# Optimization experiments

Measured on AMD Instinct MI355X. Metric: run time of the kernel, lower is better.

## Reference

```python
import jax, jax.numpy as jnp
import numpy as np

FEATS = 512   # F, forced by groups=512
K = 8         # kernel_size arg (number of shifted taps)
L = 3         # lag
CK = 3        # actual Conv1d kernel width
OUT_CH = K * FEATS * L  # 12288


def setup_inputs() -> dict:
    key = jax.random.key(0)
    k1, k2, k3 = jax.random.split(key, 3)
    M, T = 4, 1024
    x = jax.random.normal(k1, (M, T, FEATS), dtype=jnp.float32)
    # grouped conv: out_channels=12288, in_channels/groups = 512/512 = 1, width 3
    conv_w = jax.random.normal(k2, (OUT_CH, 1, CK), dtype=jnp.float32) * 0.1
    conv_b = jax.random.normal(k3, (OUT_CH,), dtype=jnp.float32) * 0.1
    return {"x": x, "conv_w": conv_w, "conv_b": conv_b}


def reference(x, conv_w, conv_b):
    M, T, F = x.shape
    # causal grouped conv: left-pad CK-1, feature_group_count = F
    xc = jnp.transpose(x, (0, 2, 1))  # (M, F, T)
    y = jax.lax.conv_general_dilated(
        xc, conv_w, window_strides=(1,), padding=[(CK - 1, 0)],
        dimension_numbers=("NCH", "OIH", "NCH"), feature_group_count=F)
    y = y + conv_b[None, :, None]                   # (M, OUT_CH, T)
    y = jnp.transpose(y, (0, 2, 1)).reshape(M, T, F, K, L)

    t = jnp.arange(T)
    lag_slices = []
    for l in range(L):
        taps = []
        for i in range(K):
            s = i + l
            # NOTE: original torch code rolls along the FEATURE axis (dim 2 of (M,T,F))
            z = jnp.roll(y[:, :, :, i, l], s, axis=2)      # (M, T, F)
            # ... but zeros the first s TIME steps (faithful reproduction)
            z = jnp.where((t >= s)[None, :, None], z, 0.0)
            taps.append(z)
        lag_slices.append(jnp.stack(taps, axis=-1))        # (M, T, F, K)
    x_new = jnp.stack(lag_slices, axis=0)                   # (L, M, T, F, K)
    x_new = x_new.reshape(L * M, T, F, K)
    return jnp.transpose(x_new, (2, 1, 0, 3))               # (F, T, L*M, K)
```

## Files before the change

### kernel.cpp

```cpp
#include <hip/hip_runtime.h>


typedef float f32x4 __attribute__((ext_vector_type(4)));

#define NF 512
#define NT 1024
#define TT 64
#define XROW 12
#define NROWS 66
#define XM 808

__global__ __launch_bounds__(256) void caconv_kernel(
    const float* __restrict__ x,
    const float* __restrict__ w,
    const float* __restrict__ b,
    float* __restrict__ out)
{
    __shared__ float x_lds[4 * XM];
    __shared__ float w_lds[72];
    __shared__ float b_lds[24];

    const int tid = threadIdx.x;
    const int f   = blockIdx.x >> 4;
    const int t0  = (blockIdx.x & 15) * TT;

    if (tid < 72) {
        const int l = tid / 24, r = tid - l * 24, tap = r >> 3, k = r & 7;
        const int fs = (f - k - l + NF) & (NF - 1);
        w_lds[tid] = w[(fs * 24 + k * 3 + l) * 3 + tap];
    } else if (tid < 96) {
        const int j = tid - 72, l = j >> 3, k = j & 7;
        const int fs = (f - k - l + NF) & (NF - 1);
        b_lds[j] = b[fs * 24 + k * 3 + l];
    }

    for (int i = tid; i < 4 * NROWS * XROW; i += 256) {
        const int fi  = i % 12;
        const int row = i / 12;
        const int tt  = row % NROWS;
        const int m   = row / NROWS;
        const int tg  = t0 - 2 + tt;
        const int fs  = (f - 11 + fi + NF) & (NF - 1);
        float v = 0.0f;
        if (tg >= 0) v = x[((m << 10) + tg) * NF + fs];
        x_lds[m * XM + tt * XROW + fi] = v;
    }
    __syncthreads();

    float* const outb = out + ((size_t)f * NT + t0) * 96;

    const int kh = tid & 1;
    const int k0 = kh << 2;
    int q     = tid >> 1;
    int t_off = q / 12;
    int lm    = q - t_off * 12;

#pragma unroll 1
    for (int j = 0; j < 6; ++j) {
        const int l = lm >> 2, m = lm & 3;

        const float* wp = w_lds + l * 24 + k0;
        const f32x4 w0 = *(const f32x4*)(wp);
        const f32x4 w1 = *(const f32x4*)(wp + 8);
        const f32x4 w2 = *(const f32x4*)(wp + 16);
        f32x4 acc = *(const f32x4*)(b_lds + l * 8 + k0);

        const float* xp = x_lds + m * XM + t_off * XROW + (8 - l - k0);

        {
            const float r0 = xp[0], r1 = xp[1], r2 = xp[2], r3 = xp[3];
            acc[0] += w0[0] * r3; acc[1] += w0[1] * r2;
            acc[2] += w0[2] * r1; acc[3] += w0[3] * r0;
        }
        {
            const float r0 = xp[12], r1 = xp[13], r2 = xp[14], r3 = xp[15];
            acc[0] += w1[0] * r3; acc[1] += w1[1] * r2;
            acc[2] += w1[2] * r1; acc[3] += w1[3] * r0;
        }
        {
            const float r0 = xp[24], r1 = xp[25], r2 = xp[26], r3 = xp[27];
            acc[0] += w2[0] * r3; acc[1] += w2[1] * r2;
            acc[2] += w2[2] * r1; acc[3] += w2[3] * r0;
        }

        if (t0 == 0 && t_off < 9) {
#pragma unroll
            for (int kk = 0; kk < 4; ++kk)
                if (t_off < k0 + kk + l) acc[kk] = 0.0f;
        }

        *(f32x4*)(outb + (t_off * 12 + lm) * 8 + k0) = acc;

        lm += 8; t_off += 10;
        if (lm >= 12) { lm -= 12; ++t_off; }
    }
}

extern "C" void kernel_launch(void* const* d_in, const int* in_sizes, int n_in,
                              void* d_out, int out_size, void* d_ws, size_t ws_size,
                              hipStream_t stream)
{
    const float* x = (const float*)d_in[0];
    const float* w = (const float*)d_in[1];
    const float* b = (const float*)d_in[2];
    float* out = (float*)d_out;

    const int grid = NF * (NT / TT);
    caconv_kernel<<<grid, 256, 0, stream>>>(x, w, b, out);
}
```

Measured before the change: 48.21 us.

## Make blocks persistent over time tiles with double-buffered register-prefetched staging

Each block now covers 512 time steps as 8 tiles instead of one 64-step tile, which shrinks the grid from 8192 to 1024 blocks. The next tile's x window is prefetched into registers while the current tile is computed from a double-buffered LDS slab. The staged feature window is narrowed from 12 to 10 columns and the gather addresses are precomputed once per block. The aim is to hide global load latency behind compute and to amortize per-block weight and bias setup, at the cost of fewer blocks in flight and more registers.

```diff
diff --git a/kernel.cpp b/kernel.cpp
--- a/kernel.cpp
+++ b/kernel.cpp
@@ -6,93 +6,135 @@
 #define NF 512
 #define NT 1024
 #define TT 64
-#define XROW 12
+#define XROW 10
 #define NROWS 66
-#define XM 808
+#define XM 668
+#define SLAB (4 * XM)
+#define NSTG (4 * NROWS * XROW)
+#define NIT 11
+#define DUMMY (SLAB - 1)
 
-__global__ __launch_bounds__(256) void caconv_kernel(
+__global__ __launch_bounds__(256, 4) void caconv_kernel(
     const float* __restrict__ x,
     const float* __restrict__ w,
     const float* __restrict__ b,
     float* __restrict__ out)
 {
-    __shared__ float x_lds[4 * XM];
+    __shared__ float x_lds[2 * SLAB];
     __shared__ float w_lds[72];
     __shared__ float b_lds[24];
 
-    const int tid = threadIdx.x;
-    const int f   = blockIdx.x >> 4;
-    const int t0  = (blockIdx.x & 15) * TT;
+    const int tid   = threadIdx.x;
+    const int f     = blockIdx.x >> 1;
+    const int tbase = (blockIdx.x & 1) << 9;
 
     if (tid < 72) {
-        const int l = tid / 24, r = tid - l * 24, tap = r >> 3, k = r & 7;
+        const int l = tid / 24, rr = tid - l * 24, tap = rr >> 3, k = rr & 7;
         const int fs = (f - k - l + NF) & (NF - 1);
         w_lds[tid] = w[(fs * 24 + k * 3 + l) * 3 + tap];
     } else if (tid < 96) {
-        const int j = tid - 72, l = j >> 3, k = j & 7;
+        const int jj = tid - 72, l = jj >> 3, k = jj & 7;
         const int fs = (f - k - l + NF) & (NF - 1);
-        b_lds[j] = b[fs * 24 + k * 3 + l];
+        b_lds[jj] = b[fs * 24 + k * 3 + l];
     }
 
-    for (int i = tid; i < 4 * NROWS * XROW; i += 256) {
-        const int fi  = i % 12;
-        const int row = i / 12;
-        const int tt  = row % NROWS;
-        const int m   = row / NROWS;
-        const int tg  = t0 - 2 + tt;
-        const int fs  = (f - 11 + fi + NF) & (NF - 1);
+    int goff[NIT], pk[NIT];
+#pragma unroll
+    for (int it = 0; it < NIT; ++it) {
+        const int i = tid + it * 256;
+        if (i < NSTG) {
+            const int fi = i % 10, row = i / 10;
+            const int tt = row % 66, m = row / 66;
+            const int fs = (f - 9 + fi + NF) & (NF - 1);
+            goff[it] = ((tt - 2) << 9) + fs;
+            pk[it]   = ((m * XM + tt * XROW + fi) << 2) | m;
+        } else {
+            goff[it] = -(1 << 30);
+            pk[it]   = DUMMY << 2;
+        }
+    }
+
+    float r[NIT];
+
+#pragma unroll
+    for (int it = 0; it < NIT; ++it) {
+        const int g = goff[it] + (tbase << 9);
         float v = 0.0f;
-        if (tg >= 0) v = x[((m << 10) + tg) * NF + fs];
-        x_lds[m * XM + tt * XROW + fi] = v;
+        if (g >= 0) v = x[g + ((pk[it] & 3) << 19)];
+        r[it] = v;
     }
+#pragma unroll
+    for (int it = 0; it < NIT; ++it) x_lds[pk[it] >> 2] = r[it];
     __syncthreads();
 
-    float* const outb = out + ((size_t)f * NT + t0) * 96;
-
-    const int kh = tid & 1;
-    const int k0 = kh << 2;
-    int q     = tid >> 1;
-    int t_off = q / 12;
-    int lm    = q - t_off * 12;
+    const int k0     = (tid & 1) << 2;
+    const int q0     = tid >> 1;
+    const int t_off0 = q0 / 12;
+    const int lm0    = q0 - t_off0 * 12;
 
 #pragma unroll 1
-    for (int j = 0; j < 6; ++j) {
-        const int l = lm >> 2, m = lm & 3;
+    for (int j = 0; j < 8; ++j) {
+        const int t0 = tbase + j * TT;
+        const float* bufr = x_lds + (j & 1) * SLAB;
+        float* bufw       = x_lds + ((j & 1) ^ 1) * SLAB;
 
-        const float* wp = w_lds + l * 24 + k0;
-        const f32x4 w0 = *(const f32x4*)(wp);
-        const f32x4 w1 = *(const f32x4*)(wp + 8);
-        const f32x4 w2 = *(const f32x4*)(wp + 16);
-        f32x4 acc = *(const f32x4*)(b_lds + l * 8 + k0);
-
-        const float* xp = x_lds + m * XM + t_off * XROW + (8 - l - k0);
-
-        {
-            const float r0 = xp[0], r1 = xp[1], r2 = xp[2], r3 = xp[3];
-            acc[0] += w0[0] * r3; acc[1] += w0[1] * r2;
-            acc[2] += w0[2] * r1; acc[3] += w0[3] * r0;
-        }
-        {
-            const float r0 = xp[12], r1 = xp[13], r2 = xp[14], r3 = xp[15];
-            acc[0] += w1[0] * r3; acc[1] += w1[1] * r2;
-            acc[2] += w1[2] * r1; acc[3] += w1[3] * r0;
-        }
-        {
-            const float r0 = xp[24], r1 = xp[25], r2 = xp[26], r3 = xp[27];
-            acc[0] += w2[0] * r3; acc[1] += w2[1] * r2;
-            acc[2] += w2[2] * r1; acc[3] += w2[3] * r0;
+        if (j < 7) {
+            const int t1s = (t0 + TT) << 9;
+#pragma unroll
+            for (int it = 0; it < NIT; ++it) {
+                const int g = goff[it] + t1s;
+                float v = 0.0f;
+                if (g >= 0) v = x[g + ((pk[it] & 3) << 19)];
+                r[it] = v;
+            }
         }
 
-        if (t0 == 0 && t_off < 9) {
+        float* const outb = out + (size_t)((f << 10) + t0) * 96;
+        int t_off = t_off0, lm = lm0;
+#pragma unroll 1
+        for (int c = 0; c < 6; ++c) {
+            const int l = lm >> 2, m = lm & 3;
+
+            const float* wp = w_lds + l * 24 + k0;
+            const f32x4 w0 = *(const f32x4*)(wp);
+            const f32x4 w1 = *(const f32x4*)(wp + 8);
+            const f32x4 w2 = *(const f32x4*)(wp + 16);
+            f32x4 acc = *(const f32x4*)(b_lds + l * 8 + k0);
+
+            const float* xp = bufr + m * XM + t_off * XROW + (6 - l - k0);
+            {
+                const float r0 = xp[0], r1 = xp[1], r2 = xp[2], r3 = xp[3];
+                acc[0] += w0[0] * r3; acc[1] += w0[1] * r2;
+                acc[2] += w0[2] * r1; acc[3] += w0[3] * r0;
+            }
+            {
+                const float r0 = xp[10], r1 = xp[11], r2 = xp[12], r3 = xp[13];
+                acc[0] += w1[0] * r3; acc[1] += w1[1] * r2;
+                acc[2] += w1[2] * r1; acc[3] += w1[3] * r0;
+            }
+            {
+                const float r0 = xp[20], r1 = xp[21], r2 = xp[22], r3 = xp[23];
+                acc[0] += w2[0] * r3; acc[1] += w2[1] * r2;
+                acc[2] += w2[2] * r1; acc[3] += w2[3] * r0;
+            }
+
+            if (t0 == 0 && t_off < 9) {
 #pragma unroll
-            for (int kk = 0; kk < 4; ++kk)
-                if (t_off < k0 + kk + l) acc[kk] = 0.0f;
+                for (int kk = 0; kk < 4; ++kk)
+                    if (t_off < k0 + kk + l) acc[kk] = 0.0f;
+            }
+
+            *(f32x4*)(outb + (t_off * 12 + lm) * 8 + k0) = acc;
+
+            lm += 8; t_off += 10;
+            if (lm >= 12) { lm -= 12; ++t_off; }
         }
 
-        *(f32x4*)(outb + (t_off * 12 + lm) * 8 + k0) = acc;
-
-        lm += 8; t_off += 10;
-        if (lm >= 12) { lm -= 12; ++t_off; }
+        if (j < 7) {
+#pragma unroll
+            for (int it = 0; it < NIT; ++it) bufw[pk[it] >> 2] = r[it];
+            __syncthreads();
+        }
     }
 }
 
@@ -105,6 +147,6 @@
     const float* b = (const float*)d_in[2];
     float* out = (float*)d_out;
 
-    const int grid = NF * (NT / TT);
+    const int grid = NF * 2;
     caconv_kernel<<<grid, 256, 0, stream>>>(x, w, b, out);
 }
```

Result: slower. 50.21 us (+4.2%).

## Tile blocks over 8 features and slide a register window along time

Applied to the files above, without the earlier changes.

Each block now handles 8 features and 32 time steps instead of 1 feature and 64 steps. The x slab is shared across the features, so it is re-read from global memory far less often. Each thread keeps its weights and bias in registers and walks the time axis with a rolling three-row window, which drops the repeated LDS loads. The output stores shift from contiguous per-warp writes to strided 96-float steps per thread, and the grid and block shapes change.

```diff
diff --git a/kernel.cpp b/kernel.cpp
--- a/kernel.cpp
+++ b/kernel.cpp
@@ -5,94 +5,98 @@
 
 #define NF 512
 #define NT 1024
-#define TT 64
-#define XROW 12
-#define NROWS 66
-#define XM 808
+#define FB 8
+#define TT 32
+#define XROW 17
+#define NROWS (TT + 2)
+#define XM (NROWS * XROW)
+#define SLAB (4 * XM)
 
-__global__ __launch_bounds__(256) void caconv_kernel(
+__global__ __launch_bounds__(192) void caconv_kernel(
     const float* __restrict__ x,
     const float* __restrict__ w,
     const float* __restrict__ b,
     float* __restrict__ out)
 {
-    __shared__ float x_lds[4 * XM];
-    __shared__ float w_lds[72];
-    __shared__ float b_lds[24];
+    __shared__ float x_lds[SLAB];
+    __shared__ float w_lds[FB * 72];
+    __shared__ float b_lds[FB * 24];
 
     const int tid = threadIdx.x;
-    const int f   = blockIdx.x >> 4;
-    const int t0  = (blockIdx.x & 15) * TT;
+    const int f0  = (blockIdx.x >> 5) * FB;
+    const int t0  = (blockIdx.x & 31) * TT;
 
-    if (tid < 72) {
-        const int l = tid / 24, r = tid - l * 24, tap = r >> 3, k = r & 7;
-        const int fs = (f - k - l + NF) & (NF - 1);
-        w_lds[tid] = w[(fs * 24 + k * 3 + l) * 3 + tap];
-    } else if (tid < 96) {
-        const int j = tid - 72, l = j >> 3, k = j & 7;
-        const int fs = (f - k - l + NF) & (NF - 1);
-        b_lds[j] = b[fs * 24 + k * 3 + l];
+    for (int i = tid; i < FB * 96; i += 192) {
+        if (i < FB * 72) {
+            const int fl = i / 72, r = i - fl * 72;
+            const int l = r / 24, r2 = r - l * 24, tap = r2 >> 3, k = r2 & 7;
+            const int fs = (f0 + fl - k - l + NF) & (NF - 1);
+            w_lds[i] = w[(fs * 24 + k * 3 + l) * 3 + tap];
+        } else {
+            const int j = i - FB * 72;
+            const int fl = j / 24, r = j - fl * 24, l = r >> 3, k = r & 7;
+            const int fs = (f0 + fl - k - l + NF) & (NF - 1);
+            b_lds[j] = b[fs * 24 + k * 3 + l];
+        }
     }
 
-    for (int i = tid; i < 4 * NROWS * XROW; i += 256) {
-        const int fi  = i % 12;
-        const int row = i / 12;
+    for (int i = tid; i < SLAB; i += 192) {
+        const int fi  = i % XROW;
+        const int row = i / XROW;
         const int tt  = row % NROWS;
         const int m   = row / NROWS;
         const int tg  = t0 - 2 + tt;
-        const int fs  = (f - 11 + fi + NF) & (NF - 1);
+        const int fs  = (f0 - 9 + fi + NF) & (NF - 1);
         float v = 0.0f;
         if (tg >= 0) v = x[((m << 10) + tg) * NF + fs];
         x_lds[m * XM + tt * XROW + fi] = v;
     }
     __syncthreads();
 
-    float* const outb = out + ((size_t)f * NT + t0) * 96;
+    const int fl = tid / 24;
+    const int u  = tid - fl * 24;
+    const int lm = u >> 1;
+    const int k0 = (u & 1) << 2;
+    const int l  = lm >> 2;
+    const int m  = lm & 3;
+    const int fib = fl + 6 - l - k0;
 
-    const int kh = tid & 1;
-    const int k0 = kh << 2;
-    int q     = tid >> 1;
-    int t_off = q / 12;
-    int lm    = q - t_off * 12;
+    const float* wp = w_lds + fl * 72 + l * 24 + k0;
+    const f32x4 w0 = *(const f32x4*)(wp);
+    const f32x4 w1 = *(const f32x4*)(wp + 8);
+    const f32x4 w2 = *(const f32x4*)(wp + 16);
+    const f32x4 bias = *(const f32x4*)(b_lds + fl * 24 + l * 8 + k0);
 
-#pragma unroll 1
-    for (int j = 0; j < 6; ++j) {
-        const int l = lm >> 2, m = lm & 3;
+    const float* xp = x_lds + m * XM + fib;
+    float* outp = out + ((size_t)(f0 + fl) * NT + t0) * 96 + lm * 8 + k0;
 
-        const float* wp = w_lds + l * 24 + k0;
-        const f32x4 w0 = *(const f32x4*)(wp);
-        const f32x4 w1 = *(const f32x4*)(wp + 8);
-        const f32x4 w2 = *(const f32x4*)(wp + 16);
-        f32x4 acc = *(const f32x4*)(b_lds + l * 8 + k0);
+    f32x4 rA, rB, rC;
+    rA[0] = xp[0];  rA[1] = xp[1];  rA[2] = xp[2];  rA[3] = xp[3];
+    rB[0] = xp[XROW]; rB[1] = xp[XROW+1]; rB[2] = xp[XROW+2]; rB[3] = xp[XROW+3];
 
-        const float* xp = x_lds + m * XM + t_off * XROW + (8 - l - k0);
+#pragma unroll 4
+    for (int t_off = 0; t_off < TT; ++t_off) {
+        const float* rp = xp + (t_off + 2) * XROW;
+        rC[0] = rp[0]; rC[1] = rp[1]; rC[2] = rp[2]; rC[3] = rp[3];
 
-        {
-            const float r0 = xp[0], r1 = xp[1], r2 = xp[2], r3 = xp[3];
-            acc[0] += w0[0] * r3; acc[1] += w0[1] * r2;
-            acc[2] += w0[2] * r1; acc[3] += w0[3] * r0;
-        }
-        {
-            const float r0 = xp[12], r1 = xp[13], r2 = xp[14], r3 = xp[15];
-            acc[0] += w1[0] * r3; acc[1] += w1[1] * r2;
-            acc[2] += w1[2] * r1; acc[3] += w1[3] * r0;
-        }
-        {
-            const float r0 = xp[24], r1 = xp[25], r2 = xp[26], r3 = xp[27];
-            acc[0] += w2[0] * r3; acc[1] += w2[1] * r2;
-            acc[2] += w2[2] * r1; acc[3] += w2[3] * r0;
-        }
+        f32x4 acc = bias;
+        acc[0] += w0[0] * rA[3]; acc[1] += w0[1] * rA[2];
+        acc[2] += w0[2] * rA[1]; acc[3] += w0[3] * rA[0];
+        acc[0] += w1[0] * rB[3]; acc[1] += w1[1] * rB[2];
+        acc[2] += w1[2] * rB[1]; acc[3] += w1[3] * rB[0];
+        acc[0] += w2[0] * rC[3]; acc[1] += w2[1] * rC[2];
+        acc[2] += w2[2] * rC[1]; acc[3] += w2[3] * rC[0];
 
-        if (t0 == 0 && t_off < 9) {
+        if (t0 == 0 && t_off < 10) {
 #pragma unroll
             for (int kk = 0; kk < 4; ++kk)
                 if (t_off < k0 + kk + l) acc[kk] = 0.0f;
         }
 
-        *(f32x4*)(outb + (t_off * 12 + lm) * 8 + k0) = acc;
+        *(f32x4*)outp = acc;
+        outp += 96;
 
-        lm += 8; t_off += 10;
-        if (lm >= 12) { lm -= 12; ++t_off; }
+        rA = rB; rB = rC;
     }
 }
 
@@ -105,6 +109,6 @@
     const float* b = (const float*)d_in[2];
     float* out = (float*)d_out;
 
-    const int grid = NF * (NT / TT);
-    caconv_kernel<<<grid, 256, 0, stream>>>(x, w, b, out);
+    const int grid = (NF / FB) * (NT / TT);
+    caconv_kernel<<<grid, 192, 0, stream>>>(x, w, b, out);
 }
```

After: 40.90 us. 1.18x faster.
